# Kernel tuning notes

Hardware: AMD Instinct MI355X
Metric: run time of the kernel (lower is better)

The kernel has to match this reference:

```python
import jax, jax.numpy as jnp
import numpy as np

K, B, S, D, V, H = 4, 64, 50, 256, 40000, 4
DH = D // H
TOPK = 2
NEG = -1e9
SCALE = float(1.0 / np.sqrt(DH))


def setup_inputs() -> dict:
    key = jax.random.key(0)
    ks = jax.random.split(key, 16)
    s = 0.05
    return {
        "ids":   jax.random.randint(ks[0], (K, B, S), 0, V),
        "items": jax.random.randint(ks[1], (K, B, S), 0, V),
        "adj":   jax.random.randint(ks[2], (B, S, S), 0, 5),
        "alias": jax.random.randint(ks[3], (B, S), 0, S),
        "eps":   jax.random.normal(ks[4], (B, S, K), jnp.float32),
        "emb":   jax.random.normal(ks[5], (K, V, D), jnp.float32) * s,
        "agg_a": jax.random.normal(ks[6], (K, 4, D), jnp.float32) * s,
        "Wq": jax.random.normal(ks[7], (K, D, D), jnp.float32) * s,
        "Wk": jax.random.normal(ks[8], (K, D, D), jnp.float32) * s,
        "Wv": jax.random.normal(ks[9], (K, D, D), jnp.float32) * s,
        "Wo": jax.random.normal(ks[10], (K, D, D), jnp.float32) * s,
        "ln1_g": jnp.ones((K, D), jnp.float32),
        "ln1_b": jnp.zeros((K, D), jnp.float32),
        "W1": jax.random.normal(ks[11], (K, D, 4 * D), jnp.float32) * s,
        "W2": jax.random.normal(ks[12], (K, 4 * D, D), jnp.float32) * s,
        "ln2_g": jnp.ones((K, D), jnp.float32),
        "ln2_b": jnp.zeros((K, D), jnp.float32),
        "Wg": jax.random.normal(ks[13], (D, K), jnp.float32) * s,
        "Wn": jax.random.normal(ks[14], (D, K), jnp.float32) * s,
    }


def _layer_norm(x, g, b):
    m = jnp.mean(x, -1, keepdims=True)
    v = jnp.var(x, -1, keepdims=True)
    return (x - m) * jax.lax.rsqrt(v + 1e-5) * g + b


def _per_key(ids, items, emb, a, Wq, Wk, Wv, Wo, g1, b1, W1, W2, g2, b2, adj, alias):
    hg = emb[items]                                          # [B,S,D] graph-node embeddings
    # LocalAggregator: relation-typed pairwise attention over session graph (adj in {1..4})
    e = jnp.einsum('bid,bjd,rd->rbij', hg, hg, a)            # [4,B,S,S], avoids [B,S,S,D]
    e = jax.nn.leaky_relu(e, 0.2)
    alpha = jnp.full(adj.shape, NEG, e.dtype)
    for r in range(4):
        alpha = jnp.where(adj == r + 1, e[r], alpha)
    alpha = jax.nn.softmax(alpha, -1)
    h_local = jnp.einsum('bij,bjd->bid', alpha, hg)          # graph aggregation
    h = jnp.take_along_axis(h_local, alias[..., None], axis=1)   # distribute graph rows to sequence
    # memory-transformer block (pre-LN causal MHA + FFN)
    x = _layer_norm(h, g1, b1)
    q = (x @ Wq).reshape(B, S, H, DH)
    k = (x @ Wk).reshape(B, S, H, DH)
    v = (x @ Wv).reshape(B, S, H, DH)
    scores = jnp.einsum('bihd,bjhd->bhij', q, k) * SCALE
    causal = jnp.tril(jnp.ones((S, S), bool))
    scores = jnp.where(causal, scores, NEG)
    attn = jax.nn.softmax(scores, -1)
    o = jnp.einsum('bhij,bjhd->bihd', attn, v).reshape(B, S, D) @ Wo
    h = h + o
    y = _layer_norm(h, g2, b2)
    h = h + jax.nn.gelu(y @ W1) @ W2
    return h


def reference(ids, items, adj, alias, eps, emb, agg_a, Wq, Wk, Wv, Wo,
              ln1_g, ln1_b, W1, W2, ln2_g, ln2_b, Wg, Wn):
    per_key = jax.vmap(_per_key, in_axes=(0,) * 14 + (None, None))
    h_keys = per_key(ids, items, emb, agg_a, Wq, Wk, Wv, Wo,
                     ln1_g, ln1_b, W1, W2, ln2_g, ln2_b, adj, alias)   # [K,B,S,D]
    # gate input: mean over per-key input-sequence embeddings (h_seq in original)
    h_seq = jax.vmap(lambda e, i: e[i])(emb, ids).mean(0)              # [B,S,D]
    # noisy top-k gating over node-type experts
    logits = h_seq @ Wg + jax.nn.softplus(h_seq @ Wn) * eps            # [B,S,K]
    top_v, top_i = jax.lax.top_k(logits, TOPK)
    w = jax.nn.softmax(top_v, -1)                                      # [B,S,TOPK]
    gates = jnp.sum(jax.nn.one_hot(top_i, K, dtype=w.dtype) * w[..., None], axis=-2)  # [B,S,K]
    return jnp.einsum('bsk,kbsd->bsd', gates, h_keys)
```

## Files before the change

### kernel.cpp

```cpp
#include <hip/hip_runtime.h>
#include <hip/hip_bf16.h>
#include <math.h>

#define K_ 4
#define B_ 64
#define S_ 50
#define D_ 256
#define V_ 40000
#define H_ 4
#define DH_ 64
#define NEG_ (-1e9f)
#define SCALE_ 0.125f

typedef __attribute__((ext_vector_type(8))) __bf16 bf16x8v;
typedef __attribute__((ext_vector_type(4))) float f32x4v;

__device__ __forceinline__ float wred_sum(float v) {
#pragma unroll
  for (int off = 32; off > 0; off >>= 1) v += __shfl_xor(v, off, 64);
  return v;
}
__device__ __forceinline__ float wred_max(float v) {
#pragma unroll
  for (int off = 32; off > 0; off >>= 1) v = fmaxf(v, __shfl_xor(v, off, 64));
  return v;
}
__device__ __forceinline__ float softplusf(float x) {
  return (x > 20.f) ? x : log1pf(expf(x));
}
__device__ __forceinline__ float geluf(float x) {
  const float c = 0.7978845608028654f;
  float x3 = x * x * x;
  return 0.5f * x * (1.f + tanhf(c * (x + 0.044715f * x3)));
}
__device__ __forceinline__ float bf2f(unsigned int u) {
  return __uint_as_float(u << 16);
}
__device__ __forceinline__ unsigned short f2bf(float f) {
  unsigned u = __float_as_uint(f);
  return (unsigned short)((u + 0x7fffu + ((u >> 16) & 1u)) >> 16);
}
__device__ __forceinline__ void unp8(uint4 a, float* d) {
  d[0] = bf2f(a.x & 0xffffu); d[1] = bf2f(a.x >> 16);
  d[2] = bf2f(a.y & 0xffffu); d[3] = bf2f(a.y >> 16);
  d[4] = bf2f(a.z & 0xffffu); d[5] = bf2f(a.z >> 16);
  d[6] = bf2f(a.w & 0xffffu); d[7] = bf2f(a.w >> 16);
}
__device__ __forceinline__ bf16x8v cvt8(float4 a, float4 b) {
  bf16x8v r;
  r[0] = (__bf16)a.x; r[1] = (__bf16)a.y; r[2] = (__bf16)a.z; r[3] = (__bf16)a.w;
  r[4] = (__bf16)b.x; r[5] = (__bf16)b.y; r[6] = (__bf16)b.z; r[7] = (__bf16)b.w;
  return r;
}

__global__ __launch_bounds__(256) void cast_weights(
    const float* __restrict__ wq, const float* __restrict__ wk,
    const float* __restrict__ wv, const float* __restrict__ wo,
    const float* __restrict__ w1, const float* __restrict__ w2,
    unsigned short* __restrict__ wqkv, unsigned short* __restrict__ wob,
    unsigned short* __restrict__ w1b, unsigned short* __restrict__ w2b) {
  long i4 = ((long)blockIdx.x * 256 + threadIdx.x) * 4;
  const float* src;
  unsigned short* dst;
  if (i4 < 786432) {
    int sect = (int)(i4 / 262144);
    long e = i4 - (long)sect * 262144;
    src = (sect == 0) ? wq : (sect == 1) ? wk : wv;
    int k = (int)(e >> 16);
    int rem = (int)(e & 65535);
    int d = rem >> 8, n = rem & 255;
    float4 v = *(const float4*)(src + e);
    ushort4 o;
    o.x = f2bf(v.x); o.y = f2bf(v.y); o.z = f2bf(v.z); o.w = f2bf(v.w);
    *(ushort4*)(wqkv + (long)k * 196608 + (long)d * 768 + sect * 256 + n) = o;
    return;
  }
  long e;
  if (i4 < 1048576) { src = wo; e = i4 - 786432; dst = wob; }
  else if (i4 < 2097152) { src = w1; e = i4 - 1048576; dst = w1b; }
  else { src = w2; e = i4 - 2097152; dst = w2b; }
  float4 v = *(const float4*)(src + e);
  ushort4 o;
  o.x = f2bf(v.x); o.y = f2bf(v.y); o.z = f2bf(v.z); o.w = f2bf(v.w);
  *(ushort4*)(dst + e) = o;
}

__global__ __launch_bounds__(256) void gate_kernel(
    const int* __restrict__ ids, const float* __restrict__ emb,
    const float* __restrict__ Wg, const float* __restrict__ Wn,
    const float* __restrict__ eps, float* __restrict__ gates) {
  int w = threadIdx.x >> 6, lane = threadIdx.x & 63;
  int item = blockIdx.x * 4 + w;
  int b = item / S_, s = item % S_;
  int d0 = lane * 4;
  float4 hs = make_float4(0.f, 0.f, 0.f, 0.f);
#pragma unroll
  for (int k = 0; k < K_; ++k) {
    int id = ids[(k * B_ + b) * S_ + s];
    const float4 e = *(const float4*)(emb + ((long)k * V_ + id) * D_ + d0);
    hs.x += e.x; hs.y += e.y; hs.z += e.z; hs.w += e.w;
  }
  hs.x *= 0.25f; hs.y *= 0.25f; hs.z *= 0.25f; hs.w *= 0.25f;
  float logit[4];
#pragma unroll
  for (int j = 0; j < K_; ++j) {
    float pg = hs.x * Wg[(d0 + 0) * K_ + j] + hs.y * Wg[(d0 + 1) * K_ + j] +
               hs.z * Wg[(d0 + 2) * K_ + j] + hs.w * Wg[(d0 + 3) * K_ + j];
    float pn = hs.x * Wn[(d0 + 0) * K_ + j] + hs.y * Wn[(d0 + 1) * K_ + j] +
               hs.z * Wn[(d0 + 2) * K_ + j] + hs.w * Wn[(d0 + 3) * K_ + j];
    pg = wred_sum(pg);
    pn = wred_sum(pn);
    logit[j] = pg + softplusf(pn) * eps[item * K_ + j];
  }
  if (lane == 0) {
    int i0 = 0; float v0 = logit[0];
    for (int j = 1; j < K_; ++j) if (logit[j] > v0) { v0 = logit[j]; i0 = j; }
    int i1 = -1; float v1 = 0.f;
    for (int j = 0; j < K_; ++j)
      if (j != i0 && (i1 < 0 || logit[j] > v1)) { v1 = logit[j]; i1 = j; }
    float w0 = 1.f / (1.f + expf(v1 - v0));
    float w1 = 1.f - w0;
#pragma unroll
    for (int j = 0; j < K_; ++j)
      gates[item * K_ + j] = (j == i0) ? w0 : ((j == i1) ? w1 : 0.f);
  }
}

__global__ __launch_bounds__(256) void local_agg4(
    const int* __restrict__ items, const int* __restrict__ adj,
    const float* __restrict__ emb, const float* __restrict__ agg_a,
    float* __restrict__ h_raw) {
  __shared__ __bf16 hgb[64][264];
  __shared__ float e_f[50][68];
  __shared__ __bf16 alp[64][72];
  __shared__ unsigned char adj_s[64][64];
  __shared__ __bf16 a_sb[4][264];
  int kb = blockIdx.x;
  int k = kb >> 6, b = kb & 63;
  int t = threadIdx.x;
  for (int c = t; c < 2048; c += 256) {
    int row = c >> 5, c8 = (c & 31) * 8;
    bf16x8v val;
    if (row < S_) {
      int g = items[kb * S_ + row];
      const float* src = emb + ((long)k * V_ + g) * D_ + c8;
      val = cvt8(*(const float4*)src, *(const float4*)(src + 4));
    } else {
#pragma unroll
      for (int e = 0; e < 8; ++e) val[e] = (__bf16)0.f;
    }
    *(bf16x8v*)&hgb[row][c8] = val;
  }
  if (t < 128) {
    int row = t >> 5, c8 = (t & 31) * 8;
    const float* src = agg_a + ((long)k * 4 + row) * D_ + c8;
    *(bf16x8v*)&a_sb[row][c8] = cvt8(*(const float4*)src, *(const float4*)(src + 4));
  }
  for (int c = t; c < 4096; c += 256) {
    int i = c >> 6, j = c & 63;
    adj_s[i][j] = (i < S_ && j < S_)
                      ? (unsigned char)adj[((long)b * S_ + i) * S_ + j] : 0;
  }
  __syncthreads();
  int w = t >> 6, lane = t & 63;
  int m16 = lane & 15, quad = lane >> 4;
  float e_sel[4][4];
#pragma unroll
  for (int nt = 0; nt < 4; ++nt)
#pragma unroll
    for (int rg = 0; rg < 4; ++rg) e_sel[nt][rg] = NEG_;
#pragma unroll
  for (int r = 0; r < 4; ++r) {
    f32x4v acc[4];
#pragma unroll
    for (int nt = 0; nt < 4; ++nt) acc[nt] = (f32x4v){0.f, 0.f, 0.f, 0.f};
#pragma unroll
    for (int k0 = 0; k0 < 8; ++k0) {
      int kc = k0 * 32 + quad * 8;
      bf16x8v hr = *(const bf16x8v*)&hgb[w * 16 + m16][kc];
      bf16x8v ar = *(const bf16x8v*)&a_sb[r][kc];
      bf16x8v af;
#pragma unroll
      for (int e = 0; e < 8; ++e) af[e] = (__bf16)((float)hr[e] * (float)ar[e]);
#pragma unroll
      for (int nt = 0; nt < 4; ++nt) {
        bf16x8v bf = *(const bf16x8v*)&hgb[nt * 16 + m16][kc];
        acc[nt] = __builtin_amdgcn_mfma_f32_16x16x32_bf16(af, bf, acc[nt], 0, 0, 0);
      }
    }
#pragma unroll
    for (int nt = 0; nt < 4; ++nt)
#pragma unroll
      for (int rg = 0; rg < 4; ++rg) {
        int i = w * 16 + quad * 4 + rg, j = nt * 16 + m16;
        if (adj_s[i][j] == r + 1) {
          float v = acc[nt][rg];
          e_sel[nt][rg] = (v >= 0.f) ? v : 0.2f * v;
        }
      }
  }
#pragma unroll
  for (int nt = 0; nt < 4; ++nt)
#pragma unroll
    for (int rg = 0; rg < 4; ++rg) {
      int i = w * 16 + quad * 4 + rg;
      if (i < S_) e_f[i][nt * 16 + m16] = e_sel[nt][rg];
    }
  __syncthreads();
  for (int i = w; i < S_; i += 4) {
    float val = (lane < S_) ? e_f[i][lane] : -INFINITY;
    float m = wred_max(val);
    float p = expf(val - m);
    float ssum = wred_sum(p);
    alp[i][lane] = (__bf16)(p / ssum);
  }
  __syncthreads();
#pragma unroll 4
  for (int nt = 0; nt < 16; ++nt) {
    f32x4v acc = (f32x4v){0.f, 0.f, 0.f, 0.f};
#pragma unroll
    for (int k0 = 0; k0 < 2; ++k0) {
      int jb = k0 * 32 + quad * 8;
      bf16x8v af = *(const bf16x8v*)&alp[w * 16 + m16][jb];
      bf16x8v bf;
#pragma unroll
      for (int tt = 0; tt < 8; ++tt) bf[tt] = hgb[jb + tt][nt * 16 + m16];
      acc = __builtin_amdgcn_mfma_f32_16x16x32_bf16(af, bf, acc, 0, 0, 0);
    }
#pragma unroll
    for (int rg = 0; rg < 4; ++rg) {
      int i = w * 16 + quad * 4 + rg;
      if (i < S_)
        h_raw[((long)kb * S_ + i) * D_ + nt * 16 + m16] = acc[rg];
    }
  }
}

__global__ __launch_bounds__(256) void gather_ln(
    const float* __restrict__ h_raw, const int* __restrict__ alias_,
    float* __restrict__ hbuf, unsigned short* __restrict__ xb,
    const float* __restrict__ g, const float* __restrict__ bta) {
  int kb = blockIdx.x;
  int k = kb >> 6, b = kb & 63;
  int w = threadIdx.x >> 6, lane = threadIdx.x & 63;
  for (int s = w; s < S_; s += 4) {
    int src = alias_[b * S_ + s];
    const float4 v = *(const float4*)(h_raw + ((long)kb * S_ + src) * D_ + lane * 4);
    long off = ((long)kb * S_ + s) * D_ + lane * 4;
    *(float4*)(hbuf + off) = v;
    float sum = wred_sum(v.x + v.y + v.z + v.w);
    float sq = wred_sum(v.x * v.x + v.y * v.y + v.z * v.z + v.w * v.w);
    float mean = sum * (1.f / D_);
    float var = sq * (1.f / D_) - mean * mean;
    float rs = rsqrtf(var + 1e-5f);
    const float4 gv = *(const float4*)(g + k * D_ + lane * 4);
    const float4 bv = *(const float4*)(bta + k * D_ + lane * 4);
    ushort4 o;
    o.x = f2bf((v.x - mean) * rs * gv.x + bv.x);
    o.y = f2bf((v.y - mean) * rs * gv.y + bv.y);
    o.z = f2bf((v.z - mean) * rs * gv.z + bv.z);
    o.w = f2bf((v.w - mean) * rs * gv.w + bv.w);
    *(ushort4*)(xb + off) = o;
  }
}

__global__ __launch_bounds__(256) void ln_bf16(
    const float* __restrict__ x, unsigned short* __restrict__ y,
    const float* __restrict__ g, const float* __restrict__ bta) {
  int w = threadIdx.x >> 6, lane = threadIdx.x & 63;
  long row = (long)blockIdx.x * 4 + w;
  int k = (int)(row / (B_ * S_));
  const float4 v = *(const float4*)(x + row * D_ + lane * 4);
  float sum = wred_sum(v.x + v.y + v.z + v.w);
  float sq = wred_sum(v.x * v.x + v.y * v.y + v.z * v.z + v.w * v.w);
  float mean = sum * (1.f / D_);
  float var = sq * (1.f / D_) - mean * mean;
  float rs = rsqrtf(var + 1e-5f);
  const float4 gv = *(const float4*)(g + k * D_ + lane * 4);
  const float4 bv = *(const float4*)(bta + k * D_ + lane * 4);
  ushort4 o;
  o.x = f2bf((v.x - mean) * rs * gv.x + bv.x);
  o.y = f2bf((v.y - mean) * rs * gv.y + bv.y);
  o.z = f2bf((v.z - mean) * rs * gv.z + bv.z);
  o.w = f2bf((v.w - mean) * rs * gv.w + bv.w);
  *(ushort4*)(y + row * D_ + lane * 4) = o;
}

__global__ __launch_bounds__(256) void bgemm(
    const unsigned short* __restrict__ A, const unsigned short* __restrict__ B,
    long strideA, long strideB, int N, int Kd,
    float* __restrict__ Cf, long strideCf,
    const float* __restrict__ R, long strideR,
    unsigned short* __restrict__ Cb, long strideCb, int act) {
  __shared__ unsigned short sA[64][40];
  __shared__ unsigned short sB[64][40];
  int z = blockIdx.z;
  A += (long)z * strideA;
  B += (long)z * strideB;
  int t = threadIdx.x, w = t >> 6, lane = t & 63;
  int row0 = blockIdx.x * 64, col0 = blockIdx.y * 64;
  f32x4v acc[4];
#pragma unroll
  for (int nt = 0; nt < 4; ++nt) acc[nt] = (f32x4v){0.f, 0.f, 0.f, 0.f};
  int ar = t >> 2, ac = (t & 3) * 8;
  int bk = t >> 3, bn = (t & 7) * 8;
  int m16 = lane & 15, kg = (lane >> 4) * 8;
  for (int k0 = 0; k0 < Kd; k0 += 32) {
    uint4 av = *(const uint4*)(A + (long)(row0 + ar) * Kd + k0 + ac);
    uint4 bv = *(const uint4*)(B + (long)(k0 + bk) * N + col0 + bn);
    __syncthreads();
    *(uint4*)&sA[ar][ac] = av;
    sB[bn + 0][bk] = (unsigned short)(bv.x & 0xffffu);
    sB[bn + 1][bk] = (unsigned short)(bv.x >> 16);
    sB[bn + 2][bk] = (unsigned short)(bv.y & 0xffffu);
    sB[bn + 3][bk] = (unsigned short)(bv.y >> 16);
    sB[bn + 4][bk] = (unsigned short)(bv.z & 0xffffu);
    sB[bn + 5][bk] = (unsigned short)(bv.z >> 16);
    sB[bn + 6][bk] = (unsigned short)(bv.w & 0xffffu);
    sB[bn + 7][bk] = (unsigned short)(bv.w >> 16);
    __syncthreads();
    bf16x8v af = *(const bf16x8v*)&sA[w * 16 + m16][kg];
#pragma unroll
    for (int nt = 0; nt < 4; ++nt) {
      bf16x8v bf = *(const bf16x8v*)&sB[nt * 16 + m16][kg];
      acc[nt] = __builtin_amdgcn_mfma_f32_16x16x32_bf16(af, bf, acc[nt], 0, 0, 0);
    }
  }
  int rbase = row0 + w * 16 + (lane >> 4) * 4;
  int cb = lane & 15;
#pragma unroll
  for (int nt = 0; nt < 4; ++nt) {
#pragma unroll
    for (int i2 = 0; i2 < 4; ++i2) {
      long off = (long)(rbase + i2) * N + col0 + nt * 16 + cb;
      float vv = acc[nt][i2];
      if (R) vv += R[(long)z * strideR + off];
      if (act == 1) vv = geluf(vv);
      if (Cf) Cf[(long)z * strideCf + off] = vv;
      if (Cb) Cb[(long)z * strideCb + off] = f2bf(vv);
    }
  }
}

__global__ __launch_bounds__(256) void attn_kernel(
    const unsigned short* __restrict__ qkv, unsigned short* __restrict__ o) {
  __shared__ float qs[S_][65], ks[S_][65], vs[S_][65];
  int idx = blockIdx.x;
  int h = idx & 3;
  int kb = idx >> 2;
  long base = (long)kb * S_ * 768;
  int t = threadIdx.x;
  for (int f = t; f < S_ * 8; f += 256) {
    int row = f >> 3, c8 = (f & 7) * 8;
    long g = base + (long)row * 768 + h * DH_ + c8;
    unp8(*(const uint4*)(qkv + g), &qs[row][c8]);
    unp8(*(const uint4*)(qkv + g + 256), &ks[row][c8]);
    unp8(*(const uint4*)(qkv + g + 512), &vs[row][c8]);
  }
  __syncthreads();
  int w = t >> 6, lane = t & 63;
  for (int i = w; i < S_; i += 4) {
    int jj = (lane < S_) ? lane : 0;
    float dot = 0.f;
#pragma unroll
    for (int d = 0; d < DH_; ++d) dot = fmaf(qs[i][d], ks[jj][d], dot);
    float val = (lane <= i) ? dot * SCALE_ : ((lane < S_) ? NEG_ : -INFINITY);
    float m = wred_max(val);
    float p = expf(val - m);
    float ssum = wred_sum(p);
    float pr = p / ssum;
    float acc = 0.f;
    for (int j = 0; j <= i; ++j)
      acc = fmaf(__shfl(pr, j, 64), vs[j][lane], acc);
    o[((long)kb * S_ + i) * D_ + h * DH_ + lane] = f2bf(acc);
  }
}

__global__ __launch_bounds__(256) void combine_kernel(
    const float* __restrict__ gates, const float* __restrict__ h,
    float* __restrict__ out) {
  int w = threadIdx.x >> 6, lane = threadIdx.x & 63;
  int item = blockIdx.x * 4 + w;
  float g0 = gates[item * 4 + 0], g1 = gates[item * 4 + 1];
  float g2 = gates[item * 4 + 2], g3 = gates[item * 4 + 3];
  long off = (long)item * D_ + lane * 4;
  const long PK = (long)B_ * S_ * D_;
  float4 a = *(const float4*)(h + off);
  float4 b = *(const float4*)(h + PK + off);
  float4 c = *(const float4*)(h + 2 * PK + off);
  float4 d = *(const float4*)(h + 3 * PK + off);
  float4 o;
  o.x = g0 * a.x + g1 * b.x + g2 * c.x + g3 * d.x;
  o.y = g0 * a.y + g1 * b.y + g2 * c.y + g3 * d.y;
  o.z = g0 * a.z + g1 * b.z + g2 * c.z + g3 * d.z;
  o.w = g0 * a.w + g1 * b.w + g2 * c.w + g3 * d.w;
  *(float4*)(out + off) = o;
}

extern "C" void kernel_launch(void* const* d_in, const int* in_sizes, int n_in,
                              void* d_out, int out_size, void* d_ws,
                              size_t ws_size, hipStream_t stream) {
  const int* ids = (const int*)d_in[0];
  const int* items = (const int*)d_in[1];
  const int* adj = (const int*)d_in[2];
  const int* alias = (const int*)d_in[3];
  const float* eps = (const float*)d_in[4];
  const float* emb = (const float*)d_in[5];
  const float* agg_a = (const float*)d_in[6];
  const float* Wq = (const float*)d_in[7];
  const float* Wk = (const float*)d_in[8];
  const float* Wv = (const float*)d_in[9];
  const float* Wo = (const float*)d_in[10];
  const float* ln1g = (const float*)d_in[11];
  const float* ln1b = (const float*)d_in[12];
  const float* W1 = (const float*)d_in[13];
  const float* W2 = (const float*)d_in[14];
  const float* ln2g = (const float*)d_in[15];
  const float* ln2b = (const float*)d_in[16];
  const float* Wg = (const float*)d_in[17];
  const float* Wn = (const float*)d_in[18];
  float* out = (float*)d_out;

  const long BSD = (long)B_ * S_ * D_;
  float* ws = (float*)d_ws;
  float* gates = ws;
  float* hbuf = ws + 16384;
  unsigned short* ub = (unsigned short*)(ws + 16384 + 4 * BSD);
  unsigned short* xb = ub;
  unsigned short* qkvb = ub + 3276800;
  unsigned short* tb = qkvb;
  float* h_raw = (float*)qkvb;
  unsigned short* wqkvb = ub + 16384000;
  unsigned short* wob = wqkvb + 2359296;
  unsigned short* w1b = wob + 262144;
  unsigned short* w2b = w1b + 1048576;

  const long DD = 65536, DH4 = 262144, T4 = 3276800;

  cast_weights<<<3072, 256, 0, stream>>>(Wq, Wk, Wv, Wo, W1, W2,
                                         wqkvb, wob, w1b, w2b);
  gate_kernel<<<800, 256, 0, stream>>>(ids, emb, Wg, Wn, eps, gates);
  local_agg4<<<256, 256, 0, stream>>>(items, adj, emb, agg_a, h_raw);
  gather_ln<<<256, 256, 0, stream>>>(h_raw, alias, hbuf, xb, ln1g, ln1b);
  bgemm<<<dim3(50, 12, 4), 256, 0, stream>>>(xb, wqkvb, BSD, 196608, 768, 256,
      (float*)0, 0, (const float*)0, 0, qkvb, 2457600, 0);
  attn_kernel<<<K_ * B_ * H_, 256, 0, stream>>>(qkvb, xb);
  bgemm<<<dim3(50, 4, 4), 256, 0, stream>>>(xb, wob, BSD, DD, 256, 256,
      hbuf, BSD, hbuf, BSD, (unsigned short*)0, 0, 0);
  ln_bf16<<<3200, 256, 0, stream>>>(hbuf, xb, ln2g, ln2b);
  bgemm<<<dim3(50, 16, 4), 256, 0, stream>>>(xb, w1b, BSD, DH4, 1024, 256,
      (float*)0, 0, (const float*)0, 0, tb, T4, 1);
  bgemm<<<dim3(50, 4, 4), 256, 0, stream>>>(tb, w2b, T4, DH4, 256, 1024,
      hbuf, BSD, hbuf, BSD, (unsigned short*)0, 0, 0);
  combine_kernel<<<800, 256, 0, stream>>>(gates, hbuf, out);
}
```

Before: 492.3 us.

## Pre-transpose bf16 weights and use K-major B tiles with register prefetch

The weight cast now writes each matrix in transposed, N-major bf16 layout. The GEMM can then load B tiles with vectorized 16-byte stores into shared memory instead of scattering individual shorts. The GEMM also doubles the K step to 64 and prefetches the next tile into registers while the current one is computed, cutting barriers per K and hiding global latency. The transposing cast writes strided scalar shorts, which is less coalesced, but it runs once per call on small weights. The wqkvT offset is also changed from 2359296 to 786432, which matches the actual size of the packed QKV weight.

New measurement: 441.2 us. 1.12x faster.

```diff
diff --git a/kernel.cpp b/kernel.cpp
--- a/kernel.cpp
+++ b/kernel.cpp
@@ -57,32 +57,50 @@
     const float* __restrict__ wq, const float* __restrict__ wk,
     const float* __restrict__ wv, const float* __restrict__ wo,
     const float* __restrict__ w1, const float* __restrict__ w2,
-    unsigned short* __restrict__ wqkv, unsigned short* __restrict__ wob,
-    unsigned short* __restrict__ w1b, unsigned short* __restrict__ w2b) {
+    unsigned short* __restrict__ wqkvT, unsigned short* __restrict__ woT,
+    unsigned short* __restrict__ w1T, unsigned short* __restrict__ w2T) {
   long i4 = ((long)blockIdx.x * 256 + threadIdx.x) * 4;
-  const float* src;
-  unsigned short* dst;
   if (i4 < 786432) {
     int sect = (int)(i4 / 262144);
     long e = i4 - (long)sect * 262144;
-    src = (sect == 0) ? wq : (sect == 1) ? wk : wv;
-    int k = (int)(e >> 16);
-    int rem = (int)(e & 65535);
+    const float* src = (sect == 0) ? wq : (sect == 1) ? wk : wv;
+    int k = (int)(e >> 16), rem = (int)(e & 65535);
     int d = rem >> 8, n = rem & 255;
     float4 v = *(const float4*)(src + e);
-    ushort4 o;
-    o.x = f2bf(v.x); o.y = f2bf(v.y); o.z = f2bf(v.z); o.w = f2bf(v.w);
-    *(ushort4*)(wqkv + (long)k * 196608 + (long)d * 768 + sect * 256 + n) = o;
+    unsigned short* base = wqkvT + ((long)k * 768 + sect * 256 + n) * 256 + d;
+    base[0] = f2bf(v.x); base[256] = f2bf(v.y);
+    base[512] = f2bf(v.z); base[768] = f2bf(v.w);
     return;
   }
-  long e;
-  if (i4 < 1048576) { src = wo; e = i4 - 786432; dst = wob; }
-  else if (i4 < 2097152) { src = w1; e = i4 - 1048576; dst = w1b; }
-  else { src = w2; e = i4 - 2097152; dst = w2b; }
-  float4 v = *(const float4*)(src + e);
-  ushort4 o;
-  o.x = f2bf(v.x); o.y = f2bf(v.y); o.z = f2bf(v.z); o.w = f2bf(v.w);
-  *(ushort4*)(dst + e) = o;
+  if (i4 < 1048576) {
+    long e = i4 - 786432;
+    int k = (int)(e >> 16), rem = (int)(e & 65535);
+    int d = rem >> 8, n = rem & 255;
+    float4 v = *(const float4*)(wo + e);
+    unsigned short* base = woT + ((long)k * 256 + n) * 256 + d;
+    base[0] = f2bf(v.x); base[256] = f2bf(v.y);
+    base[512] = f2bf(v.z); base[768] = f2bf(v.w);
+    return;
+  }
+  if (i4 < 2097152) {
+    long e = i4 - 1048576;
+    int k = (int)(e >> 18), rem = (int)(e & 262143);
+    int d = rem >> 10, n = rem & 1023;
+    float4 v = *(const float4*)(w1 + e);
+    unsigned short* base = w1T + ((long)k * 1024 + n) * 256 + d;
+    base[0] = f2bf(v.x); base[256] = f2bf(v.y);
+    base[512] = f2bf(v.z); base[768] = f2bf(v.w);
+    return;
+  }
+  {
+    long e = i4 - 2097152;
+    int k = (int)(e >> 18), rem = (int)(e & 262143);
+    int d = rem >> 8, n = rem & 255;
+    float4 v = *(const float4*)(w2 + e);
+    unsigned short* base = w2T + ((long)k * 256 + n) * 1024 + d;
+    base[0] = f2bf(v.x); base[1024] = f2bf(v.y);
+    base[2048] = f2bf(v.z); base[3072] = f2bf(v.w);
+  }
 }
 
 __global__ __launch_bounds__(256) void gate_kernel(
@@ -286,48 +304,56 @@
   *(ushort4*)(y + row * D_ + lane * 4) = o;
 }
 
-__global__ __launch_bounds__(256) void bgemm(
-    const unsigned short* __restrict__ A, const unsigned short* __restrict__ B,
-    long strideA, long strideB, int N, int Kd,
+__global__ __launch_bounds__(256) void bgemm2(
+    const unsigned short* __restrict__ A, const unsigned short* __restrict__ Bt,
+    long strideA, long strideBt, int N, int Kd,
     float* __restrict__ Cf, long strideCf,
     const float* __restrict__ R, long strideR,
     unsigned short* __restrict__ Cb, long strideCb, int act) {
-  __shared__ unsigned short sA[64][40];
-  __shared__ unsigned short sB[64][40];
+  __shared__ unsigned short sA[64][72];
+  __shared__ unsigned short sB[64][72];
   int z = blockIdx.z;
   A += (long)z * strideA;
-  B += (long)z * strideB;
+  Bt += (long)z * strideBt;
   int t = threadIdx.x, w = t >> 6, lane = t & 63;
   int row0 = blockIdx.x * 64, col0 = blockIdx.y * 64;
+  int m16 = lane & 15, quad = lane >> 4;
   f32x4v acc[4];
 #pragma unroll
   for (int nt = 0; nt < 4; ++nt) acc[nt] = (f32x4v){0.f, 0.f, 0.f, 0.f};
-  int ar = t >> 2, ac = (t & 3) * 8;
-  int bk = t >> 3, bn = (t & 7) * 8;
-  int m16 = lane & 15, kg = (lane >> 4) * 8;
-  for (int k0 = 0; k0 < Kd; k0 += 32) {
-    uint4 av = *(const uint4*)(A + (long)(row0 + ar) * Kd + k0 + ac);
-    uint4 bv = *(const uint4*)(B + (long)(k0 + bk) * N + col0 + bn);
+  int sr = t >> 2, sc = (t & 3) * 16;
+  const unsigned short* pa = A + (long)(row0 + sr) * Kd + sc;
+  const unsigned short* pb = Bt + (long)(col0 + sr) * Kd + sc;
+  uint4 a0 = *(const uint4*)(pa);
+  uint4 a1 = *(const uint4*)(pa + 8);
+  uint4 b0 = *(const uint4*)(pb);
+  uint4 b1 = *(const uint4*)(pb + 8);
+  for (int k0 = 0; k0 < Kd; k0 += 64) {
     __syncthreads();
-    *(uint4*)&sA[ar][ac] = av;
-    sB[bn + 0][bk] = (unsigned short)(bv.x & 0xffffu);
-    sB[bn + 1][bk] = (unsigned short)(bv.x >> 16);
-    sB[bn + 2][bk] = (unsigned short)(bv.y & 0xffffu);
-    sB[bn + 3][bk] = (unsigned short)(bv.y >> 16);
-    sB[bn + 4][bk] = (unsigned short)(bv.z & 0xffffu);
-    sB[bn + 5][bk] = (unsigned short)(bv.z >> 16);
-    sB[bn + 6][bk] = (unsigned short)(bv.w & 0xffffu);
-    sB[bn + 7][bk] = (unsigned short)(bv.w >> 16);
+    *(uint4*)&sA[sr][sc] = a0;
+    *(uint4*)&sA[sr][sc + 8] = a1;
+    *(uint4*)&sB[sr][sc] = b0;
+    *(uint4*)&sB[sr][sc + 8] = b1;
+    if (k0 + 64 < Kd) {
+      a0 = *(const uint4*)(pa + k0 + 64);
+      a1 = *(const uint4*)(pa + k0 + 72);
+      b0 = *(const uint4*)(pb + k0 + 64);
+      b1 = *(const uint4*)(pb + k0 + 72);
+    }
     __syncthreads();
-    bf16x8v af = *(const bf16x8v*)&sA[w * 16 + m16][kg];
-#pragma unroll
-    for (int nt = 0; nt < 4; ++nt) {
-      bf16x8v bf = *(const bf16x8v*)&sB[nt * 16 + m16][kg];
-      acc[nt] = __builtin_amdgcn_mfma_f32_16x16x32_bf16(af, bf, acc[nt], 0, 0, 0);
-    }
-  }
-  int rbase = row0 + w * 16 + (lane >> 4) * 4;
-  int cb = lane & 15;
+#pragma unroll
+    for (int half = 0; half < 2; ++half) {
+      int kg = half * 32 + quad * 8;
+      bf16x8v af = *(const bf16x8v*)&sA[w * 16 + m16][kg];
+#pragma unroll
+      for (int nt = 0; nt < 4; ++nt) {
+        bf16x8v bf = *(const bf16x8v*)&sB[nt * 16 + m16][kg];
+        acc[nt] = __builtin_amdgcn_mfma_f32_16x16x32_bf16(af, bf, acc[nt], 0, 0, 0);
+      }
+    }
+  }
+  int rbase = row0 + w * 16 + quad * 4;
+  int cb = m16;
 #pragma unroll
   for (int nt = 0; nt < 4; ++nt) {
 #pragma unroll
@@ -430,27 +456,27 @@
   unsigned short* qkvb = ub + 3276800;
   unsigned short* tb = qkvb;
   float* h_raw = (float*)qkvb;
-  unsigned short* wqkvb = ub + 16384000;
-  unsigned short* wob = wqkvb + 2359296;
-  unsigned short* w1b = wob + 262144;
-  unsigned short* w2b = w1b + 1048576;
-
-  const long DD = 65536, DH4 = 262144, T4 = 3276800;
+  unsigned short* wqkvT = ub + 16384000;
+  unsigned short* woT = wqkvT + 786432;
+  unsigned short* w1T = woT + 262144;
+  unsigned short* w2T = w1T + 1048576;
+
+  const long T4 = 3276800;
 
   cast_weights<<<3072, 256, 0, stream>>>(Wq, Wk, Wv, Wo, W1, W2,
-                                         wqkvb, wob, w1b, w2b);
+                                         wqkvT, woT, w1T, w2T);
   gate_kernel<<<800, 256, 0, stream>>>(ids, emb, Wg, Wn, eps, gates);
   local_agg4<<<256, 256, 0, stream>>>(items, adj, emb, agg_a, h_raw);
   gather_ln<<<256, 256, 0, stream>>>(h_raw, alias, hbuf, xb, ln1g, ln1b);
-  bgemm<<<dim3(50, 12, 4), 256, 0, stream>>>(xb, wqkvb, BSD, 196608, 768, 256,
+  bgemm2<<<dim3(50, 12, 4), 256, 0, stream>>>(xb, wqkvT, BSD, 196608, 768, 256,
       (float*)0, 0, (const float*)0, 0, qkvb, 2457600, 0);
   attn_kernel<<<K_ * B_ * H_, 256, 0, stream>>>(qkvb, xb);
-  bgemm<<<dim3(50, 4, 4), 256, 0, stream>>>(xb, wob, BSD, DD, 256, 256,
+  bgemm2<<<dim3(50, 4, 4), 256, 0, stream>>>(xb, woT, BSD, 65536, 256, 256,
       hbuf, BSD, hbuf, BSD, (unsigned short*)0, 0, 0);
   ln_bf16<<<3200, 256, 0, stream>>>(hbuf, xb, ln2g, ln2b);
-  bgemm<<<dim3(50, 16, 4), 256, 0, stream>>>(xb, w1b, BSD, DH4, 1024, 256,
+  bgemm2<<<dim3(50, 16, 4), 256, 0, stream>>>(xb, w1T, BSD, 262144, 1024, 256,
       (float*)0, 0, (const float*)0, 0, tb, T4, 1);
-  bgemm<<<dim3(50, 4, 4), 256, 0, stream>>>(tb, w2b, T4, DH4, 256, 1024,
+  bgemm2<<<dim3(50, 4, 4), 256, 0, stream>>>(tb, w2T, T4, 262144, 256, 1024,
       hbuf, BSD, hbuf, BSD, (unsigned short*)0, 0, 0);
   combine_kernel<<<800, 256, 0, stream>>>(gates, hbuf, out);
 }
```
